# Kernel optimization log

Hardware: AMD Instinct MI355X
Metric: run time of the kernel (lower is better)

The kernel has to match this reference:

```python
import jax, jax.numpy as jnp
import numpy as np

DIM = 768
NUM_HEADS = 16
HEAD_DIM = DIM // NUM_HEADS  # 48


def setup_inputs() -> dict:
    key = jax.random.key(0)
    ks = jax.random.split(key, 9)
    s = 1.0 / np.sqrt(DIM)
    return {
        "x": jax.random.normal(ks[0], (4, 2048, DIM), dtype=jnp.float32),
        "Wq": jax.random.uniform(ks[1], (DIM, DIM), jnp.float32, -s, s),
        "bq": jax.random.uniform(ks[2], (DIM,), jnp.float32, -s, s),
        "Wk": jax.random.uniform(ks[3], (DIM, DIM), jnp.float32, -s, s),
        "bk": jax.random.uniform(ks[4], (DIM,), jnp.float32, -s, s),
        "Wv": jax.random.uniform(ks[5], (DIM, DIM), jnp.float32, -s, s),
        "bv": jax.random.uniform(ks[6], (DIM,), jnp.float32, -s, s),
        "Wo": jax.random.uniform(ks[7], (DIM, DIM), jnp.float32, -s, s),
        "bo": jax.random.uniform(ks[8], (DIM,), jnp.float32, -s, s),
    }


def reference(x, Wq, bq, Wk, bk, Wv, bv, Wo, bo):
    B, S, D = x.shape
    H, Dh = NUM_HEADS, HEAD_DIM
    # qkv projections -> [B, H, S, Dh]
    q = (x @ Wq.T + bq).reshape(B, S, H, Dh).transpose(0, 2, 1, 3)
    k = (x @ Wk.T + bk).reshape(B, S, H, Dh).transpose(0, 2, 1, 3)
    v = (x @ Wv.T + bv).reshape(B, S, H, Dh).transpose(0, 2, 1, 3)
    scale = 1.0 / np.sqrt(Dh).astype(np.float32)
    scores = jnp.einsum('bhqd,bhkd->bhqk', q, k) * scale  # [B,H,S,S]
    attn = jax.nn.softmax(scores, axis=-1)
    # dropout is identity in eval mode
    out = jnp.einsum('bhqk,bhkd->bhqd', attn, v)  # [B,H,S,Dh]
    out = out.transpose(0, 2, 1, 3).reshape(B, S, D)
    return out @ Wo.T + bo
```

## Files before the change

### kernel.cpp

```cpp
#include <hip/hip_runtime.h>
#include <cstdint>
#include <cstddef>


typedef short s8v __attribute__((ext_vector_type(8)));
typedef float f4v __attribute__((ext_vector_type(4)));
typedef float f16v __attribute__((ext_vector_type(16)));

static constexpr int Bn = 4, Sn = 2048, Dn = 768, Hn = 16, DhN = 48, Dp = 64;
static constexpr int MS = Bn * Sn;

#define MFMA16(a, b, c) __builtin_amdgcn_mfma_f32_16x16x32_bf16((a), (b), (c), 0, 0, 0)
#define MFMA32(a, b, c) __builtin_amdgcn_mfma_f32_32x32x16_bf16((a), (b), (c), 0, 0, 0)

__device__ __forceinline__ int swz4(int r) { return (r + (r >> 2)) & 3; }

__device__ __forceinline__ ushort f2b(float f) {
  return (ushort)((__builtin_bit_cast(uint32_t, f) + 0x8000u) >> 16);
}
__device__ __forceinline__ uint32_t packbf(float a, float b) {
  uint32_t ua = __builtin_bit_cast(uint32_t, a) + 0x8000u;
  uint32_t ub = __builtin_bit_cast(uint32_t, b) + 0x8000u;
  return __builtin_amdgcn_perm(ub, ua, 0x07060302u);
}
__device__ __forceinline__ void pl32swap(uint32_t& a, uint32_t& b) {
  asm("v_permlane32_swap_b32 %0, %1" : "+v"(a), "+v"(b));
}
__device__ __forceinline__ float fexp2(float x) {
  return __builtin_amdgcn_exp2f(x);
}
__device__ __forceinline__ void gload_lds16(const ushort* g, ushort* l) {
  __builtin_amdgcn_global_load_lds(
      (const __attribute__((address_space(1))) uint32_t*)g,
      (__attribute__((address_space(3))) uint32_t*)l, 16, 0, 0);
}

__global__ void cvt_all(const float* __restrict__ x,
                        const float* __restrict__ wq, const float* __restrict__ wk,
                        const float* __restrict__ wv, const float* __restrict__ wo,
                        ushort* __restrict__ xb, ushort* __restrict__ wqkv,
                        ushort* __restrict__ wob) {
  const int bid = blockIdx.x;
  const float* src;
  ushort* dst;
  int i;
  if (bid < 6144) {
    src = x; dst = xb; i = bid * 256 + threadIdx.x;
  } else {
    const int r = (bid - 6144) / 576;
    i = ((bid - 6144) % 576) * 256 + threadIdx.x;
    src = (r == 0) ? wq : (r == 1) ? wk : (r == 2) ? wv : wo;
    dst = (r < 3) ? (wqkv + (size_t)r * Dn * Dn) : wob;
  }
  float4 f = ((const float4*)src)[i];
  ushort4 o = { f2b(f.x), f2b(f.y), f2b(f.z), f2b(f.w) };
  ((ushort4*)dst)[i] = o;
}

__global__ __launch_bounds__(256) void gemm_qkv(
    const ushort* __restrict__ A, const ushort* __restrict__ W,
    const float* __restrict__ bq, const float* __restrict__ bk, const float* __restrict__ bv,
    ushort* __restrict__ outq, ushort* __restrict__ outk, ushort* __restrict__ outv,
    float qscale) {
  __shared__ __align__(16) ushort As[64][64];
  __shared__ __align__(16) ushort Bs[128][64];
  const int tid = threadIdx.x, lane = tid & 63, wave = tid >> 6;
  const int l15 = lane & 15, g = lane >> 4;
  const int lin0 = blockIdx.x + blockIdx.y * 18;
  const int lin = (lin0 & 7) * 288 + (lin0 >> 3);
  const int nx = lin % 18, my = lin / 18;
  const int m0 = my * 64, n0 = nx * 128;
  const int wqm = (wave >> 1) * 64;
  const int wqx = (wave & 1) * 32;
  f4v acc[4][2] = {};

  const ushort* agp[2];
  const ushort* bgp[4];
  ushort* lap[2];
  ushort* lbp[4];
#pragma unroll
  for (int q = 0; q < 4; ++q) {
    const int slot = q * 256 + wave * 64 + lane;
    const int r = slot >> 3, sc = slot & 7;
    const int u = ((((sc & 3) ^ swz4(r & 15)) | (sc & 4)) ^ ((r & 1) << 2)) * 8;
    bgp[q] = W + (size_t)(n0 + r) * Dn + u;
    lbp[q] = &Bs[0][0] + slot * 8;
    if (q < 2) {
      agp[q] = A + (size_t)(m0 + r) * Dn + u;
      lap[q] = &As[0][0] + slot * 8;
    }
  }
  const int fcol = (g ^ swz4(l15)) * 8;
  const int par = l15 & 1;

  for (int k0 = 0; k0 < Dn; k0 += 64) {
    __syncthreads();
#pragma unroll
    for (int q = 0; q < 4; ++q) gload_lds16(bgp[q] + k0, lbp[q]);
#pragma unroll
    for (int q = 0; q < 2; ++q) gload_lds16(agp[q] + k0, lap[q]);
    __syncthreads();
#pragma unroll
    for (int h = 0; h < 2; ++h) {
      const int fc = fcol + 32 * (h ^ par);
      s8v wf[4], xf[2];
#pragma unroll
      for (int i = 0; i < 4; ++i) wf[i] = *(const s8v*)&Bs[wqm + i * 16 + l15][fc];
#pragma unroll
      for (int j = 0; j < 2; ++j) xf[j] = *(const s8v*)&As[wqx + j * 16 + l15][fc];
#pragma unroll
      for (int i = 0; i < 4; ++i)
#pragma unroll
        for (int j = 0; j < 2; ++j) acc[i][j] = MFMA16(wf[i], xf[j], acc[i][j]);
    }
  }

  const int region = nx / 6;
  const int nbase = n0 - region * 768;
  const float* bias = (region == 0) ? bq : (region == 1) ? bk : bv;
#pragma unroll
  for (int i = 0; i < 4; ++i) {
    const int n = nbase + wqm + i * 16 + g * 4;
    const float4 b4 = *(const float4*)&bias[n];
    const int h = n / DhN, dh = n - h * DhN;
#pragma unroll
    for (int j = 0; j < 2; ++j) {
      const int s = m0 + wqx + j * 16 + l15;
      const int b = s >> 11, srow = s & 2047;
      const int bh = b * Hn + h;
      float v0 = acc[i][j][0] + b4.x, v1 = acc[i][j][1] + b4.y;
      float v2 = acc[i][j][2] + b4.z, v3 = acc[i][j][3] + b4.w;
      if (region == 0) { v0 *= qscale; v1 *= qscale; v2 *= qscale; v3 *= qscale; }
      if (region < 2) {
        ushort4 o = { f2b(v0), f2b(v1), f2b(v2), f2b(v3) };
        ushort* dst = region ? outk : outq;
        *(ushort4*)&dst[((size_t)bh * Sn + srow) * Dp + dh] = o;
      } else {
        outv[((size_t)bh * DhN + dh + 0) * Sn + srow] = f2b(v0);
        outv[((size_t)bh * DhN + dh + 1) * Sn + srow] = f2b(v1);
        outv[((size_t)bh * DhN + dh + 2) * Sn + srow] = f2b(v2);
        outv[((size_t)bh * DhN + dh + 3) * Sn + srow] = f2b(v3);
      }
    }
  }
}

__global__ __launch_bounds__(256) void gemm_out(
    const ushort* __restrict__ A, const ushort* __restrict__ W,
    const float* __restrict__ bias, float* __restrict__ out) {
  __shared__ __align__(16) ushort As[64][64];
  __shared__ __align__(16) ushort Bs[128][64];
  const int tid = threadIdx.x, lane = tid & 63, wave = tid >> 6;
  const int l15 = lane & 15, g = lane >> 4;
  const int lin0 = blockIdx.x + blockIdx.y * 6;
  const int lin = (lin0 & 7) * 96 + (lin0 >> 3);
  const int nx = lin % 6, my = lin / 6;
  const int m0 = my * 64, n0 = nx * 128;
  const int wqm = (wave >> 1) * 64;
  const int wqx = (wave & 1) * 32;
  f4v acc[4][2] = {};

  const ushort* agp[2];
  const ushort* bgp[4];
  ushort* lap[2];
  ushort* lbp[4];
#pragma unroll
  for (int q = 0; q < 4; ++q) {
    const int slot = q * 256 + wave * 64 + lane;
    const int r = slot >> 3, sc = slot & 7;
    const int u = ((((sc & 3) ^ swz4(r & 15)) | (sc & 4)) ^ ((r & 1) << 2)) * 8;
    bgp[q] = W + (size_t)(n0 + r) * Dn + u;
    lbp[q] = &Bs[0][0] + slot * 8;
    if (q < 2) {
      agp[q] = A + (size_t)(m0 + r) * Dn + u;
      lap[q] = &As[0][0] + slot * 8;
    }
  }
  const int fcol = (g ^ swz4(l15)) * 8;
  const int par = l15 & 1;

  for (int k0 = 0; k0 < Dn; k0 += 64) {
    __syncthreads();
#pragma unroll
    for (int q = 0; q < 4; ++q) gload_lds16(bgp[q] + k0, lbp[q]);
#pragma unroll
    for (int q = 0; q < 2; ++q) gload_lds16(agp[q] + k0, lap[q]);
    __syncthreads();
#pragma unroll
    for (int h = 0; h < 2; ++h) {
      const int fc = fcol + 32 * (h ^ par);
      s8v wf[4], xf[2];
#pragma unroll
      for (int i = 0; i < 4; ++i) wf[i] = *(const s8v*)&Bs[wqm + i * 16 + l15][fc];
#pragma unroll
      for (int j = 0; j < 2; ++j) xf[j] = *(const s8v*)&As[wqx + j * 16 + l15][fc];
#pragma unroll
      for (int i = 0; i < 4; ++i)
#pragma unroll
        for (int j = 0; j < 2; ++j) acc[i][j] = MFMA16(wf[i], xf[j], acc[i][j]);
    }
  }

#pragma unroll
  for (int i = 0; i < 4; ++i) {
    const int n = n0 + wqm + i * 16 + g * 4;
    const float4 b4 = *(const float4*)&bias[n];
#pragma unroll
    for (int j = 0; j < 2; ++j) {
      const int s = m0 + wqx + j * 16 + l15;
      float4 o4 = { acc[i][j][0] + b4.x, acc[i][j][1] + b4.y,
                    acc[i][j][2] + b4.z, acc[i][j][3] + b4.w };
      *(float4*)&out[(size_t)s * Dn + n] = o4;
    }
  }
}

__global__ __launch_bounds__(512) void attn_fused(
    const ushort* __restrict__ qg, const ushort* __restrict__ kgl,
    const ushort* __restrict__ vg, ushort* __restrict__ og) {
  __shared__ __align__(16) ushort smem[2][7168];
  const int tid = threadIdx.x;
  const int lane = tid & 63;
  const int wave = tid >> 6;
  const int w4 = wave & 3;
  const int kg = wave >> 2;
  const int l31 = lane & 31;
  const int h = lane >> 5;
  const int lin = blockIdx.x + (blockIdx.y << 4);
  const int k8 = lin >> 3;
  const int bh = (lin & 7) * 8 + (k8 >> 4);
  const int q0 = (k8 & 15) * 128;
  const ushort* qb = qg + (size_t)bh * Sn * Dp;
  const ushort* kb = kgl + (size_t)bh * Sn * Dp + (size_t)kg * 1024 * Dp;
  const ushort* vb = vg + (size_t)bh * DhN * Sn + kg * 1024;
  ushort* KaH = &smem[kg][0];
  ushort* KbH = &smem[kg][2048];
  ushort* VsH = &smem[kg][3072];

  ((uint32_t*)&smem[0][6144])[tid] = (tid < 32) ? 0x3F803F80u : 0u;
  ((uint32_t*)&smem[1][6144])[tid] = (tid < 32) ? 0x3F803F80u : 0u;

  s8v qf[3];
#pragma unroll
  for (int kc = 0; kc < 3; ++kc)
    qf[kc] = *(const s8v*)(qb + (size_t)(q0 + w4 * 32 + l31) * Dp + kc * 16 + h * 8);

  const ushort* gsrc[3];
  ushort* ldst[3];
  int gstep[3];
#pragma unroll
  for (int t = 0; t < 3; ++t) {
    const int c = w4 + 4 * t;
    if (c < 4) {
      const int row = 16 * c + (lane >> 2), j = lane & 3;
      gsrc[t] = kb + (size_t)row * Dp + (j ^ ((row >> 1) & 3)) * 8;
      ldst[t] = KaH + 16 * c * 32 + lane * 8;
      gstep[t] = 64 * Dp;
    } else if (c < 6) {
      const int row = 32 * (c - 4) + (lane >> 1), j = lane & 1;
      gsrc[t] = kb + (size_t)row * Dp + 32 + (j ^ ((row >> 2) & 1)) * 8;
      ldst[t] = KbH + 32 * (c - 4) * 16 + lane * 8;
      gstep[t] = 64 * Dp;
    } else {
      const int row = 8 * (c - 6) + (lane >> 3), j = lane & 7;
      gsrc[t] = vb + (size_t)row * Sn + (j ^ (row & 7)) * 8;
      ldst[t] = VsH + 8 * (c - 6) * 64 + lane * 8;
      gstep[t] = 64;
    }
  }

  f16v o0 = {}, o1 = {};

  for (int kt = 0; kt < 1024; kt += 64) {
    __syncthreads();
#pragma unroll
    for (int t = 0; t < 3; ++t) {
      gload_lds16(gsrc[t], ldst[t]);
      gsrc[t] += gstep[t];
    }
    __syncthreads();

#pragma unroll
    for (int mg = 0; mg < 2; ++mg) {
      const int row = 32 * mg + l31;
      const int s1 = (l31 >> 1) & 3, s2 = (l31 >> 2) & 1;
      s8v a0 = *(const s8v*)(KaH + row * 32 + ((0 | h) ^ s1) * 8);
      s8v a1 = *(const s8v*)(KaH + row * 32 + ((2 | h) ^ s1) * 8);
      s8v a2 = *(const s8v*)(KbH + row * 16 + ((h) ^ s2) * 8);
      f16v sc = {};
      __builtin_amdgcn_s_setprio(1);
      sc = MFMA32(a0, qf[0], sc);
      sc = MFMA32(a1, qf[1], sc);
      sc = MFMA32(a2, qf[2], sc);
      __builtin_amdgcn_s_setprio(0);
      float p[16];
#pragma unroll
      for (int r = 0; r < 16; ++r) p[r] = fexp2(sc[r]);

#pragma unroll
      for (int c2 = 0; c2 < 2; ++c2) {
        const int rb = 8 * c2;
        uint32_t w0 = packbf(p[rb + 0], p[rb + 1]);
        uint32_t w1 = packbf(p[rb + 2], p[rb + 3]);
        uint32_t w2 = packbf(p[rb + 4], p[rb + 5]);
        uint32_t w3 = packbf(p[rb + 6], p[rb + 7]);
        pl32swap(w0, w2);
        pl32swap(w1, w3);
        uint4 af = { w0, w1, w2, w3 };
        const s8v pa = __builtin_bit_cast(s8v, af);
        const int kcv = 2 * mg + c2;
        const int vc = ((2 * kcv + h) ^ (l31 & 7)) * 8;
        const s8v v0 = *(const s8v*)(VsH + l31 * 64 + vc);
        const s8v v1 = *(const s8v*)(VsH + (32 + l31) * 64 + vc);
        __builtin_amdgcn_s_setprio(1);
        o0 = MFMA32(pa, v0, o0);
        o1 = MFMA32(pa, v1, o1);
        __builtin_amdgcn_s_setprio(0);
      }
    }
  }

  __syncthreads();
  float* scr = (float*)&smem[0][0];
  if (kg == 1) {
#pragma unroll
    for (int r = 0; r < 16; ++r) scr[r * 256 + w4 * 64 + lane] = o0[r];
  }
  __syncthreads();
  if (kg == 0) {
#pragma unroll
    for (int r = 0; r < 16; ++r) o0[r] += scr[r * 256 + w4 * 64 + lane];
  }
  __syncthreads();
  if (kg == 1) {
#pragma unroll
    for (int r = 0; r < 16; ++r) scr[r * 256 + w4 * 64 + lane] = o1[r];
  }
  __syncthreads();
  if (kg == 0) {
#pragma unroll
    for (int r = 0; r < 16; ++r) o1[r] += scr[r * 256 + w4 * 64 + lane];

    const int b = bh >> 4, hh = bh & 15;
#pragma unroll
    for (int r = 0; r < 16; ++r) {
      const int q = (r & 3) + 8 * (r >> 2) + 4 * h;
      const float lsum = __shfl(o1[r], 16 + (lane & 32), 64);
      const float inv = 1.0f / lsum;
      const int s = q0 + w4 * 32 + q;
      const size_t base = ((size_t)(b * Sn + s)) * Dn + hh * DhN;
      og[base + l31] = f2b(o0[r] * inv);
      if (l31 < 16) og[base + 32 + l31] = f2b(o1[r] * inv);
    }
  }
}

extern "C" void kernel_launch(void* const* d_in, const int* in_sizes, int n_in,
                              void* d_out, int out_size, void* d_ws, size_t ws_size,
                              hipStream_t stream) {
  (void)in_sizes; (void)n_in; (void)out_size; (void)ws_size;
  const float* x  = (const float*)d_in[0];
  const float* Wq = (const float*)d_in[1];
  const float* bq = (const float*)d_in[2];
  const float* Wk = (const float*)d_in[3];
  const float* bk = (const float*)d_in[4];
  const float* Wv = (const float*)d_in[5];
  const float* bv = (const float*)d_in[6];
  const float* Wo = (const float*)d_in[7];
  const float* bo = (const float*)d_in[8];

  size_t off = 0;
  auto alloc = [&](size_t bytes) {
    void* p = (char*)d_ws + off;
    off += (bytes + 255) & ~(size_t)255;
    return p;
  };
  ushort* xb    = (ushort*)alloc((size_t)MS * Dn * 2);
  ushort* Wqkvb = (ushort*)alloc((size_t)3 * Dn * Dn * 2);
  ushort* Wob   = (ushort*)alloc((size_t)Dn * Dn * 2);
  ushort* qbuf  = (ushort*)alloc((size_t)Bn * Hn * Sn * Dp * 2);
  ushort* kbuf  = (ushort*)alloc((size_t)Bn * Hn * Sn * Dp * 2);
  ushort* vbuf  = (ushort*)alloc((size_t)Bn * Hn * DhN * Sn * 2);
  ushort* ao    = (ushort*)alloc((size_t)MS * Dn * 2);

  cvt_all<<<6144 + 4 * 576, 256, 0, stream>>>(x, Wq, Wk, Wv, Wo, xb, Wqkvb, Wob);

  const dim3 blk(256);
  const float qscale = 0.20823510929813633f;
  gemm_qkv<<<dim3(18, MS / 64), blk, 0, stream>>>(xb, Wqkvb, bq, bk, bv,
                                                  qbuf, kbuf, vbuf, qscale);

  attn_fused<<<dim3(Sn / 128, Bn * Hn), dim3(512), 0, stream>>>(qbuf, kbuf, vbuf, ao);

  gemm_out<<<dim3(6, MS / 64), blk, 0, stream>>>(ao, Wob, bo, (float*)d_out);
}
```

Measured before the change: 224.8 us.

## Load V fragments directly from global memory instead of staging through LDS

```diff
diff --git a/kernel.cpp b/kernel.cpp
--- a/kernel.cpp
+++ b/kernel.cpp
@@ -215,7 +215,7 @@
   }
 }
 
-__global__ __launch_bounds__(512) void attn_fused(
+__global__ __launch_bounds__(512, 8) void attn_fused(
     const ushort* __restrict__ qg, const ushort* __restrict__ kgl,
     const ushort* __restrict__ vg, ushort* __restrict__ og) {
   __shared__ __align__(16) ushort smem[2][7168];
@@ -235,48 +235,40 @@
   const ushort* vb = vg + (size_t)bh * DhN * Sn + kg * 1024;
   ushort* KaH = &smem[kg][0];
   ushort* KbH = &smem[kg][2048];
-  ushort* VsH = &smem[kg][3072];
-
-  ((uint32_t*)&smem[0][6144])[tid] = (tid < 32) ? 0x3F803F80u : 0u;
-  ((uint32_t*)&smem[1][6144])[tid] = (tid < 32) ? 0x3F803F80u : 0u;
 
   s8v qf[3];
 #pragma unroll
   for (int kc = 0; kc < 3; ++kc)
     qf[kc] = *(const s8v*)(qb + (size_t)(q0 + w4 * 32 + l31) * Dp + kc * 16 + h * 8);
 
-  const ushort* gsrc[3];
-  ushort* ldst[3];
-  int gstep[3];
-#pragma unroll
-  for (int t = 0; t < 3; ++t) {
-    const int c = w4 + 4 * t;
-    if (c < 4) {
-      const int row = 16 * c + (lane >> 2), j = lane & 3;
-      gsrc[t] = kb + (size_t)row * Dp + (j ^ ((row >> 1) & 3)) * 8;
-      ldst[t] = KaH + 16 * c * 32 + lane * 8;
-      gstep[t] = 64 * Dp;
-    } else if (c < 6) {
-      const int row = 32 * (c - 4) + (lane >> 1), j = lane & 1;
-      gsrc[t] = kb + (size_t)row * Dp + 32 + (j ^ ((row >> 2) & 1)) * 8;
-      ldst[t] = KbH + 32 * (c - 4) * 16 + lane * 8;
-      gstep[t] = 64 * Dp;
-    } else {
-      const int row = 8 * (c - 6) + (lane >> 3), j = lane & 7;
-      gsrc[t] = vb + (size_t)row * Sn + (j ^ (row & 7)) * 8;
-      ldst[t] = VsH + 8 * (c - 6) * 64 + lane * 8;
-      gstep[t] = 64;
-    }
+  const ushort* vgp0 = vb + (size_t)l31 * Sn;
+  const ushort* vgp1 = vb + (size_t)(32 + l31) * Sn;
+  uint4 c1 = { 0u, 0u, 0u, 0u };
+  if (l31 == 16) c1 = (uint4){ 0x3F803F80u, 0x3F803F80u, 0x3F803F80u, 0x3F803F80u };
+  const s8v v1const = __builtin_bit_cast(s8v, c1);
+
+  const ushort* gsrc[2];
+  ushort* ldst[2];
+  {
+    const int row = 16 * w4 + (lane >> 2), j = lane & 3;
+    gsrc[0] = kb + (size_t)row * Dp + (j ^ ((row >> 1) & 3)) * 8;
+    ldst[0] = KaH + 16 * w4 * 32 + lane * 8;
+  }
+  if (w4 < 2) {
+    const int row = 32 * w4 + (lane >> 1), j = lane & 1;
+    gsrc[1] = kb + (size_t)row * Dp + 32 + (j ^ ((row >> 2) & 1)) * 8;
+    ldst[1] = KbH + 32 * w4 * 16 + lane * 8;
   }
 
   f16v o0 = {}, o1 = {};
 
   for (int kt = 0; kt < 1024; kt += 64) {
     __syncthreads();
-#pragma unroll
-    for (int t = 0; t < 3; ++t) {
-      gload_lds16(gsrc[t], ldst[t]);
-      gsrc[t] += gstep[t];
+    gload_lds16(gsrc[0], ldst[0]);
+    gsrc[0] += 64 * Dp;
+    if (w4 < 2) {
+      gload_lds16(gsrc[1], ldst[1]);
+      gsrc[1] += 64 * Dp;
     }
     __syncthreads();
 
@@ -309,9 +301,10 @@
         uint4 af = { w0, w1, w2, w3 };
         const s8v pa = __builtin_bit_cast(s8v, af);
         const int kcv = 2 * mg + c2;
-        const int vc = ((2 * kcv + h) ^ (l31 & 7)) * 8;
-        const s8v v0 = *(const s8v*)(VsH + l31 * 64 + vc);
-        const s8v v1 = *(const s8v*)(VsH + (32 + l31) * 64 + vc);
+        const int ko = kt + (2 * kcv + h) * 8;
+        const s8v v0 = *(const s8v*)(vgp0 + ko);
+        s8v v1 = v1const;
+        if (l31 < 16) v1 = *(const s8v*)(vgp1 + ko);
         __builtin_amdgcn_s_setprio(1);
         o0 = MFMA32(pa, v0, o0);
         o1 = MFMA32(pa, v1, o1);
```

After: 415.8 us. 1.85x slower.
